# Kernel tuning notes

Hardware: AMD Instinct MI355X
Metric: run time of the kernel (lower is better)

Reference implementation:

```python
import jax, jax.numpy as jnp
import numpy as np

SEQ = 4096
EMBED = 1024


def setup_inputs() -> dict:
    key = jax.random.key(0)
    k1, k2 = jax.random.split(key)
    x = jax.random.normal(k1, (SEQ, EMBED), dtype=jnp.float32)
    # torch Linear(embed, 3*embed): store transposed weight so y = x @ W + b
    W = jax.random.normal(k2, (EMBED, 3 * EMBED), dtype=jnp.float32) * (1.0 / np.sqrt(EMBED))
    b = jnp.zeros((3 * EMBED,), dtype=jnp.float32)
    return {"x": x, "W": W, "b": b}


def reference(x, W, b):
    # QKV projection: [S, 3E] -> chunk along features
    qkv = x @ W + b
    q, k, v = jnp.split(qkv, 3, axis=1)  # each [S, E]
    d = q.shape[-1]
    scale = jnp.sqrt(jnp.asarray(d, dtype=x.dtype))
    logits = (q @ k.T) / scale  # [S, S]
    S = q.shape[0]
    causal = jnp.triu(jnp.ones((S, S), dtype=bool), k=1)
    logits = jnp.where(causal, -jnp.inf, logits)
    w = jax.nn.softmax(logits, axis=1)
    return w @ v  # [S, E]
```

## Files before the change

### kernel.cpp

```cpp
#include <hip/hip_runtime.h>

typedef short s16x8 __attribute__((ext_vector_type(8)));
typedef unsigned short u16;
typedef u16 u16x8 __attribute__((ext_vector_type(8)));
typedef float f32x4 __attribute__((ext_vector_type(4)));

#define SEQ 4096
#define EMBED 1024
#define NQKV 3072

static __device__ __forceinline__ u16 f2bf(float f) {
  unsigned int u = __float_as_uint(f);
  u += 0x7fffu + ((u >> 16) & 1u);
  return (u16)(u >> 16);
}
static __device__ __forceinline__ float bf2f(u16 b) {
  return __uint_as_float(((unsigned int)b) << 16);
}

static __device__ __forceinline__ f32x4 mfma16(s16x8 a, s16x8 b, f32x4 c) {
  return __builtin_amdgcn_mfma_f32_16x16x32_bf16(a, b, c, 0, 0, 0);
}

static __device__ __forceinline__ void gl2lds(const u16* g, u16* l) {
  __builtin_amdgcn_global_load_lds(
      (const __attribute__((address_space(1))) unsigned int*)g,
      (__attribute__((address_space(3))) unsigned int*)l, 16, 0, 0);
}

#define WAITVM(n) asm volatile("s_waitcnt vmcnt(" #n ")" ::: "memory")
#define LGKM0 asm volatile("s_waitcnt lgkmcnt(0)" ::: "memory")
#define BAR() asm volatile("s_waitcnt lgkmcnt(0)\n\ts_barrier" ::: "memory")

__global__ __launch_bounds__(256) void conv_x(const float* __restrict__ x,
                                              u16* __restrict__ xbf) {
  const size_t base = ((size_t)blockIdx.x * 256 + threadIdx.x) * 16;
  u16 tmp[16];
#pragma unroll
  for (int p = 0; p < 4; ++p) {
    float4 v = *reinterpret_cast<const float4*>(&x[base + p * 4]);
    tmp[p * 4 + 0] = f2bf(v.x); tmp[p * 4 + 1] = f2bf(v.y);
    tmp[p * 4 + 2] = f2bf(v.z); tmp[p * 4 + 3] = f2bf(v.w);
  }
  *reinterpret_cast<u16x8*>(&xbf[base]) = *reinterpret_cast<u16x8*>(&tmp[0]);
  *reinterpret_cast<u16x8*>(&xbf[base + 8]) = *reinterpret_cast<u16x8*>(&tmp[8]);
}

__global__ __launch_bounds__(256) void conv_wT(const float* __restrict__ W,
                                               u16* __restrict__ wT) {
  __shared__ u16 t[64][72];
  const int n0 = blockIdx.x * 64;
  const int k0 = blockIdx.y * 64;
  const int tid = threadIdx.x;
  const int rr = tid >> 3, c8 = (tid & 7) * 8;
#pragma unroll
  for (int p = 0; p < 2; ++p) {
    int r = p * 32 + rr;
    float4 a = *reinterpret_cast<const float4*>(&W[(size_t)(k0 + r) * NQKV + n0 + c8]);
    float4 b = *reinterpret_cast<const float4*>(&W[(size_t)(k0 + r) * NQKV + n0 + c8 + 4]);
    t[r][c8 + 0] = f2bf(a.x); t[r][c8 + 1] = f2bf(a.y);
    t[r][c8 + 2] = f2bf(a.z); t[r][c8 + 3] = f2bf(a.w);
    t[r][c8 + 4] = f2bf(b.x); t[r][c8 + 5] = f2bf(b.y);
    t[r][c8 + 6] = f2bf(b.z); t[r][c8 + 7] = f2bf(b.w);
  }
  __syncthreads();
#pragma unroll
  for (int p = 0; p < 2; ++p) {
    int c = p * 32 + rr;
    u16x8 v;
#pragma unroll
    for (int j = 0; j < 8; ++j) v[j] = t[c8 + j][c];
    *reinterpret_cast<u16x8*>(&wT[(size_t)(n0 + c) * EMBED + k0 + c8]) = v;
  }
}

#define GSTAGE(dst, srcbase, stride)                                          \
  {                                                                           \
    _Pragma("unroll") for (int c_ = 0; c_ < 4; ++c_) {                        \
      gl2lds((srcbase) + (size_t)((c_ * 4 + w) * 8 + srow) * (stride) + scol, \
             (dst) + (c_ * 4 + w) * 512);                                     \
    }                                                                         \
  }

__global__ __launch_bounds__(256) void qkv_gemm(const u16* __restrict__ xbf,
                                                const u16* __restrict__ wT,
                                                const float* __restrict__ bias,
                                                u16* __restrict__ qkv) {
  __shared__ u16 As[2][8192];
  __shared__ u16 Bs[2][8192];
  const int b = blockIdx.x;
  const int bs = (b & 7) * 96 + (b >> 3);
  const int bm = bs / 24, bn = bs % 24;
  const int m0 = bm * 128, n0 = bn * 128;
  const int tid = threadIdx.x;
  const int w = tid >> 6, l = tid & 63;
  const int wr = (w >> 1) * 64, wc = (w & 1) * 64;
  const int lg = l >> 4, lr = l & 15;
  const int srow = l >> 3;
  const int scol = ((l & 7) ^ (srow & 7)) << 3;

  f32x4 acc[4][4];
#pragma unroll
  for (int i = 0; i < 4; ++i)
#pragma unroll
    for (int j = 0; j < 4; ++j) acc[i][j] = (f32x4){0.f, 0.f, 0.f, 0.f};

  const u16* xa = xbf + (size_t)m0 * EMBED;
  const u16* wb = wT + (size_t)n0 * EMBED;

  GSTAGE(As[0], xa, EMBED);
  GSTAGE(Bs[0], wb, EMBED);

  for (int t = 0; t < 16; ++t) {
    const int cur = t & 1, nx = cur ^ 1;
    if (t < 15) {
      LGKM0;
      GSTAGE(As[nx], xa + (t + 1) * 64, EMBED);
      GSTAGE(Bs[nx], wb + (t + 1) * 64, EMBED);
      WAITVM(8);
    } else {
      WAITVM(0);
    }
    BAR();
#pragma unroll
    for (int kk = 0; kk < 2; ++kk) {
      const int csw = (kk * 32 + lg * 8) ^ ((lr & 7) << 3);
      s16x8 af[4], bfr[4];
#pragma unroll
      for (int mb = 0; mb < 4; ++mb)
        af[mb] = *reinterpret_cast<const s16x8*>(&As[cur][(wr + mb * 16 + lr) * 64 + csw]);
#pragma unroll
      for (int nb = 0; nb < 4; ++nb)
        bfr[nb] = *reinterpret_cast<const s16x8*>(&Bs[cur][(wc + nb * 16 + lr) * 64 + csw]);
#pragma unroll
      for (int mb = 0; mb < 4; ++mb)
#pragma unroll
        for (int nb = 0; nb < 4; ++nb)
          acc[mb][nb] = mfma16(af[mb], bfr[nb], acc[mb][nb]);
    }
    BAR();
  }

#pragma unroll
  for (int mb = 0; mb < 4; ++mb)
#pragma unroll
    for (int nb = 0; nb < 4; ++nb) {
      const int col = n0 + wc + nb * 16 + lr;
      const float bv = bias[col];
#pragma unroll
      for (int e = 0; e < 4; ++e) {
        const int row = m0 + wr + mb * 16 + lg * 4 + e;
        qkv[(size_t)row * NQKV + col] = f2bf(acc[mb][nb][e] + bv);
      }
    }
}

__global__ __launch_bounds__(256) void v_transpose(const u16* __restrict__ qkv,
                                                   u16* __restrict__ vT) {
  __shared__ u16 t[64][72];
  const int s0 = blockIdx.x * 64;
  const int c0 = blockIdx.y * 64;
  const int tid = threadIdx.x;
  const int rr = tid >> 3, c8 = (tid & 7) * 8;
#pragma unroll
  for (int p = 0; p < 2; ++p) {
    int r = p * 32 + rr;
    *reinterpret_cast<u16x8*>(&t[r][c8]) =
        *reinterpret_cast<const u16x8*>(&qkv[(size_t)(s0 + r) * NQKV + 2 * EMBED + c0 + c8]);
  }
  __syncthreads();
#pragma unroll
  for (int p = 0; p < 2; ++p) {
    int c = p * 32 + rr;
    u16x8 v;
#pragma unroll
    for (int j = 0; j < 8; ++j) v[j] = t[c8 + j][c];
    *reinterpret_cast<u16x8*>(&vT[(size_t)(c0 + c) * SEQ + s0 + c8]) = v;
  }
}

__global__ __launch_bounds__(256) void s_gemm(const u16* __restrict__ qkv,
                                              u16* __restrict__ Sp) {
  __shared__ u16 As[2][8192];
  __shared__ u16 Bs[2][8192];
  const int b = blockIdx.x;
  const int bs = (b & 7) * 66 + (b >> 3);
  int mt = 0, cum = 0;
  while (cum + mt + 1 <= bs) { cum += mt + 1; ++mt; }
  const int nt = bs - cum;
  const int m0 = mt * 128, n0 = nt * 128;
  const int tid = threadIdx.x;
  const int w = tid >> 6, l = tid & 63;
  const int wr = (w >> 1) * 64, wc = (w & 1) * 64;
  const int lg = l >> 4, lr = l & 15;
  const int srow = l >> 3;
  const int scol = ((l & 7) ^ (srow & 7)) << 3;

  f32x4 acc[4][4];
#pragma unroll
  for (int i = 0; i < 4; ++i)
#pragma unroll
    for (int j = 0; j < 4; ++j) acc[i][j] = (f32x4){0.f, 0.f, 0.f, 0.f};

  const u16* qa = qkv + (size_t)m0 * NQKV;
  const u16* kb = qkv + (size_t)n0 * NQKV + EMBED;

  GSTAGE(As[0], qa, NQKV);
  GSTAGE(Bs[0], kb, NQKV);

  for (int t = 0; t < 16; ++t) {
    const int cur = t & 1, nx = cur ^ 1;
    if (t < 15) {
      LGKM0;
      GSTAGE(As[nx], qa + (t + 1) * 64, NQKV);
      GSTAGE(Bs[nx], kb + (t + 1) * 64, NQKV);
      WAITVM(8);
    } else {
      WAITVM(0);
    }
    BAR();
#pragma unroll
    for (int kk = 0; kk < 2; ++kk) {
      const int csw = (kk * 32 + lg * 8) ^ ((lr & 7) << 3);
      s16x8 af[4], bfr[4];
#pragma unroll
      for (int mb = 0; mb < 4; ++mb)
        af[mb] = *reinterpret_cast<const s16x8*>(&As[cur][(wr + mb * 16 + lr) * 64 + csw]);
#pragma unroll
      for (int nb = 0; nb < 4; ++nb)
        bfr[nb] = *reinterpret_cast<const s16x8*>(&Bs[cur][(wc + nb * 16 + lr) * 64 + csw]);
#pragma unroll
      for (int mb = 0; mb < 4; ++mb)
#pragma unroll
        for (int nb = 0; nb < 4; ++nb)
          acc[mb][nb] = mfma16(af[mb], bfr[nb], acc[mb][nb]);
    }
    BAR();
  }

  u16* base = Sp + (size_t)bs * 16384;
#pragma unroll
  for (int mb = 0; mb < 4; ++mb)
#pragma unroll
    for (int nb = 0; nb < 4; ++nb) {
      const int cn = wc + nb * 16 + lr;
#pragma unroll
      for (int e = 0; e < 4; ++e) {
        const int rm = wr + mb * 16 + lg * 4 + e;
        base[rm * 128 + cn] = f2bf(acc[mb][nb][e]);
      }
    }
}

__global__ __launch_bounds__(256) void softmax_rows(u16* __restrict__ Sp) {
  __shared__ float red[8];
  const int bid = blockIdx.x;
  const int tid = threadIdx.x;
  const int w = tid >> 6, l = tid & 63;
  const float NEG = -3.0e38f;

  for (int half = 0; half < 2; ++half) {
    const int r = half ? (4095 - bid) : bid;
    const int mt = r >> 7, rr = r & 127;
    const int Lp = (mt + 1) << 7;
    const size_t tri = (size_t)mt * (mt + 1) / 2;

    float v[16];
    float mx = NEG;
#pragma unroll
    for (int s = 0; s < 2; ++s) {
      const int j = tid * 8 + s * 2048;
      if (j < Lp) {
        const u16* p = Sp + (tri + (j >> 7)) * 16384 + rr * 128 + (j & 127);
        u16x8 xv = *reinterpret_cast<const u16x8*>(p);
#pragma unroll
        for (int e = 0; e < 8; ++e) {
          float f = (j + e <= r) ? bf2f(xv[e]) * 0.03125f : NEG;
          v[s * 8 + e] = f;
          mx = fmaxf(mx, f);
        }
      } else {
#pragma unroll
        for (int e = 0; e < 8; ++e) v[s * 8 + e] = NEG;
      }
    }
#pragma unroll
    for (int off = 32; off >= 1; off >>= 1) mx = fmaxf(mx, __shfl_xor(mx, off, 64));
    if (l == 0) red[w] = mx;
    __syncthreads();
    mx = fmaxf(fmaxf(red[0], red[1]), fmaxf(red[2], red[3]));

    float sum = 0.f;
#pragma unroll
    for (int i = 0; i < 16; ++i) {
      float e = __expf(v[i] - mx);
      v[i] = e;
      sum += e;
    }
#pragma unroll
    for (int off = 32; off >= 1; off >>= 1) sum += __shfl_xor(sum, off, 64);
    if (l == 0) red[4 + w] = sum;
    __syncthreads();
    sum = red[4] + red[5] + red[6] + red[7];
    const float inv = 1.f / sum;

#pragma unroll
    for (int s = 0; s < 2; ++s) {
      const int j = tid * 8 + s * 2048;
      if (j < Lp) {
        u16x8 pk;
#pragma unroll
        for (int e = 0; e < 8; ++e) pk[e] = f2bf(v[s * 8 + e] * inv);
        *reinterpret_cast<u16x8*>(Sp + (tri + (j >> 7)) * 16384 + rr * 128 + (j & 127)) = pk;
      }
    }
    __syncthreads();
  }
}

__global__ __launch_bounds__(256) void pv_gemm(const u16* __restrict__ Sp,
                                               const u16* __restrict__ vT,
                                               float* __restrict__ out) {
  __shared__ u16 As[2][8192];
  __shared__ u16 Bs[2][8192];
  const int nt = blockIdx.y;
  int s81 = blockIdx.x;
  int mt = 0, cum = 0, ls = 0;
  for (;;) {
    const int ns = (mt + 8) >> 3;
    if (s81 < cum + ns) { ls = s81 - cum; break; }
    cum += ns; ++mt;
  }
  const int m0 = mt * 128, n0 = nt * 128;
  const int k0 = ls * 1024;
  const int kext = (mt + 1) * 128;
  const int kend = (k0 + 1024 < kext) ? (k0 + 1024) : kext;
  const int ksteps = (kend - k0) >> 6;
  const size_t tri = (size_t)mt * (mt + 1) / 2;

  const int tid = threadIdx.x;
  const int w = tid >> 6, l = tid & 63;
  const int wr = (w >> 1) * 64, wc = (w & 1) * 64;
  const int lg = l >> 4, lr = l & 15;
  const int srow = l >> 3;
  const int scol = ((l & 7) ^ (srow & 7)) << 3;

  f32x4 acc[4][4];
#pragma unroll
  for (int i = 0; i < 4; ++i)
#pragma unroll
    for (int j = 0; j < 4; ++j) acc[i][j] = (f32x4){0.f, 0.f, 0.f, 0.f};

#define PA_SRC(t) (Sp + (tri + ((k0 + (t)*64) >> 7)) * 16384 + ((k0 + (t)*64) & 127))
#define PB_SRC(t) (vT + (size_t)n0 * SEQ + k0 + (t)*64)

  GSTAGE(As[0], PA_SRC(0), 128);
  GSTAGE(Bs[0], PB_SRC(0), SEQ);

  for (int t = 0; t < ksteps; ++t) {
    const int cur = t & 1, nx = cur ^ 1;
    if (t + 1 < ksteps) {
      LGKM0;
      GSTAGE(As[nx], PA_SRC(t + 1), 128);
      GSTAGE(Bs[nx], PB_SRC(t + 1), SEQ);
      WAITVM(8);
    } else {
      WAITVM(0);
    }
    BAR();
#pragma unroll
    for (int kk = 0; kk < 2; ++kk) {
      const int csw = (kk * 32 + lg * 8) ^ ((lr & 7) << 3);
      s16x8 af[4], bfr[4];
#pragma unroll
      for (int mb = 0; mb < 4; ++mb)
        af[mb] = *reinterpret_cast<const s16x8*>(&As[cur][(wr + mb * 16 + lr) * 64 + csw]);
#pragma unroll
      for (int nb = 0; nb < 4; ++nb)
        bfr[nb] = *reinterpret_cast<const s16x8*>(&Bs[cur][(wc + nb * 16 + lr) * 64 + csw]);
#pragma unroll
      for (int mb = 0; mb < 4; ++mb)
#pragma unroll
        for (int nb = 0; nb < 4; ++nb)
          acc[mb][nb] = mfma16(af[mb], bfr[nb], acc[mb][nb]);
    }
    BAR();
  }
#undef PA_SRC
#undef PB_SRC

#pragma unroll
  for (int mb = 0; mb < 4; ++mb)
#pragma unroll
    for (int nb = 0; nb < 4; ++nb) {
      const int col = n0 + wc + nb * 16 + lr;
#pragma unroll
      for (int e = 0; e < 4; ++e) {
        const int row = m0 + wr + mb * 16 + lg * 4 + e;
        unsafeAtomicAdd(&out[(size_t)row * EMBED + col], acc[mb][nb][e]);
      }
    }
}

__global__ __launch_bounds__(512) void attn_fb(const u16* __restrict__ qkv,
                                               const u16* __restrict__ vT,
                                               float* __restrict__ out) {
  __shared__ u16 q_lds[16][1032];
  __shared__ u16 kv_lds[8][3][2048];
  __shared__ u16 p_lds[16][136];
  __shared__ float redmax[8][16];
  __shared__ float redsum[8][16];
  const int bid = blockIdx.x;
  const int tid = threadIdx.x;
  const int w = tid >> 6, l = tid & 63;
  const int lg = l >> 4, lr = l & 15;

  const int sr = l >> 4;
  const int scb = (l & 15) * 16;
  const int scolA = ((scb ^ (sr << 4)) >> 1);
  const int scolB = ((scb ^ ((4 + sr) << 4)) >> 1);
  int boff[4];
#pragma unroll
  for (int kk = 0; kk < 4; ++kk)
    boff[kk] = lr * 256 + ((kk * 64 + lg * 16) ^ ((lr & 7) << 4));

  u16* kvb[3] = {&kv_lds[w][0][0], &kv_lds[w][1][0], &kv_lds[w][2][0]};

#define STAGE_K(dc, bufp)                                                     \
  {                                                                           \
    LGKM0;                                                                    \
    const u16* g0 = qkv + (size_t)(kb + w * 16 + sr) * NQKV + EMBED + (dc) * 128; \
    gl2lds(g0 + scolA, (bufp));                                               \
    gl2lds(g0 + 4 * NQKV + scolB, (bufp) + 512);                              \
    gl2lds(g0 + 8 * NQKV + scolA, (bufp) + 1024);                             \
    gl2lds(g0 + 12 * NQKV + scolB, (bufp) + 1536);                            \
  }
#define STAGE_V(j, bufp)                                                      \
  {                                                                           \
    LGKM0;                                                                    \
    const u16* g0 = vT + (size_t)((j) * 128 + w * 16 + sr) * SEQ + kb;        \
    gl2lds(g0 + scolA, (bufp));                                               \
    gl2lds(g0 + 4 * SEQ + scolB, (bufp) + 512);                               \
    gl2lds(g0 + 8 * SEQ + scolA, (bufp) + 1024);                              \
    gl2lds(g0 + 12 * SEQ + scolB, (bufp) + 1536);                             \
  }

  const int qb = bid * 16;
  __syncthreads();
#pragma unroll
  for (int p = 0; p < 4; ++p) {
    int idx = p * 512 + tid;
    int r = idx >> 7, c = (idx & 127) * 8;
    *reinterpret_cast<u16x8*>(&q_lds[r][c]) =
        *reinterpret_cast<const u16x8*>(&qkv[(size_t)(qb + r) * NQKV + c]);
  }
  __syncthreads();
  s16x8 qf[32];
#pragma unroll
  for (int kk = 0; kk < 32; ++kk)
    qf[kk] = *reinterpret_cast<const s16x8*>(&q_lds[lr][kk * 32 + lg * 8]);

  f32x4 o_acc[8];
#pragma unroll
  for (int j = 0; j < 8; ++j) o_acc[j] = (f32x4){0.f, 0.f, 0.f, 0.f};
  float m_st[4], l_st[4];
#pragma unroll
  for (int e = 0; e < 4; ++e) { m_st[e] = -__builtin_inff(); l_st[e] = 0.f; }

  const int n_it = (qb >> 7) + 1;
  for (int it = 0; it < n_it; ++it) {
    const int kb = it << 7;
    const int kcol = kb + w * 16 + lr;

    f32x4 s = (f32x4){0.f, 0.f, 0.f, 0.f};
    STAGE_K(0, kvb[0]);
    STAGE_K(1, kvb[1]);
#pragma unroll
    for (int dc = 0; dc < 8; ++dc) {
      if (dc < 6) {
        STAGE_K(dc + 2, kvb[(dc + 2) % 3]);
      } else if (dc == 6) {
        STAGE_V(0, kvb[2]);
      } else {
        STAGE_V(1, kvb[0]);
      }
      WAITVM(8);
      u16* cur = kvb[dc % 3];
#pragma unroll
      for (int kk = 0; kk < 4; ++kk) {
        s16x8 bfr = *reinterpret_cast<const s16x8*>((const char*)cur + boff[kk]);
        s = mfma16(qf[dc * 4 + kk], bfr, s);
      }
    }

    float sv[4], mx[4];
#pragma unroll
    for (int e = 0; e < 4; ++e) {
      float v = s[e] * 0.03125f;
      sv[e] = (kcol > qb + lg * 4 + e) ? -__builtin_inff() : v;
      mx[e] = sv[e];
    }
#pragma unroll
    for (int off = 1; off < 16; off <<= 1)
#pragma unroll
      for (int e = 0; e < 4; ++e) mx[e] = fmaxf(mx[e], __shfl_xor(mx[e], off, 64));
    if (lr == 0) {
#pragma unroll
      for (int e = 0; e < 4; ++e) redmax[w][lg * 4 + e] = mx[e];
    }
    BAR();

    float m_new[4], sc[4], pv[4], rs[4];
#pragma unroll
    for (int e = 0; e < 4; ++e) {
      float m = m_st[e];
#pragma unroll
      for (int ww = 0; ww < 8; ++ww) m = fmaxf(m, redmax[ww][lg * 4 + e]);
      m_new[e] = m;
      sc[e] = __expf(m_st[e] - m);
      pv[e] = __expf(sv[e] - m);
      rs[e] = pv[e];
    }
#pragma unroll
    for (int off = 1; off < 16; off <<= 1)
#pragma unroll
      for (int e = 0; e < 4; ++e) rs[e] += __shfl_xor(rs[e], off, 64);
    if (lr == 0) {
#pragma unroll
      for (int e = 0; e < 4; ++e) redsum[w][lg * 4 + e] = rs[e];
    }
#pragma unroll
    for (int e = 0; e < 4; ++e) p_lds[lg * 4 + e][w * 16 + lr] = f2bf(pv[e]);
    BAR();

#pragma unroll
    for (int e = 0; e < 4; ++e) {
      float a2 = l_st[e] * sc[e];
#pragma unroll
      for (int ww = 0; ww < 8; ++ww) a2 += redsum[ww][lg * 4 + e];
      l_st[e] = a2;
      m_st[e] = m_new[e];
    }
#pragma unroll
    for (int j = 0; j < 8; ++j)
#pragma unroll
      for (int e = 0; e < 4; ++e) o_acc[j][e] *= sc[e];

    s16x8 pa[4];
#pragma unroll
    for (int kk = 0; kk < 4; ++kk)
      pa[kk] = *reinterpret_cast<const s16x8*>(&p_lds[lr][kk * 32 + lg * 8]);

#pragma unroll
    for (int j = 0; j < 8; ++j) {
      if (j < 6) {
        STAGE_V(j + 2, kvb[(j + 4) % 3]);
        WAITVM(8);
      } else if (j == 6) {
        WAITVM(4);
      } else {
        WAITVM(0);
      }
      u16* cur = kvb[(j + 2) % 3];
#pragma unroll
      for (int kk = 0; kk < 4; ++kk) {
        s16x8 bfr = *reinterpret_cast<const s16x8*>((const char*)cur + boff[kk]);
        o_acc[j] = mfma16(pa[kk], bfr, o_acc[j]);
      }
    }
  }

#pragma unroll
  for (int j = 0; j < 8; ++j) {
    const int col = j * 128 + w * 16 + lr;
#pragma unroll
    for (int e = 0; e < 4; ++e)
      out[(size_t)(qb + lg * 4 + e) * EMBED + col] = o_acc[j][e] / l_st[e];
  }
#undef STAGE_K
#undef STAGE_V
}

extern "C" void kernel_launch(void* const* d_in, const int* in_sizes, int n_in,
                              void* d_out, int out_size, void* d_ws, size_t ws_size,
                              hipStream_t stream) {
  (void)in_sizes; (void)n_in; (void)out_size;
  const float* x = (const float*)d_in[0];
  const float* W = (const float*)d_in[1];
  const float* bias = (const float*)d_in[2];
  float* out = (float*)d_out;

  u16* qkv = (u16*)d_ws;
  u16* vT = qkv + (size_t)SEQ * NQKV;
  u16* xbf = vT;
  u16* wT = (u16*)d_out;
  u16* Sp = (u16*)((char*)d_ws + (32u << 20));

  const size_t need = (32u << 20) + (size_t)528 * 16384 * 2;

  conv_x<<<(SEQ * EMBED) / (256 * 16), 256, 0, stream>>>(x, xbf);
  conv_wT<<<dim3(NQKV / 64, EMBED / 64), 256, 0, stream>>>(W, wT);
  qkv_gemm<<<(SEQ / 128) * (NQKV / 128), 256, 0, stream>>>(xbf, wT, bias, qkv);
  v_transpose<<<dim3(SEQ / 64, EMBED / 64), 256, 0, stream>>>(qkv, vT);

  if (ws_size >= need) {
    s_gemm<<<528, 256, 0, stream>>>(qkv, Sp);
    softmax_rows<<<2048, 256, 0, stream>>>(Sp);
    hipMemsetAsync(d_out, 0, (size_t)SEQ * EMBED * sizeof(float), stream);
    pv_gemm<<<dim3(80, 8), 256, 0, stream>>>(Sp, vT, out);
  } else {
    attn_fb<<<SEQ / 16, 512, 0, stream>>>(qkv, vT, out);
  }
}
```

Baseline: 168.8 us.

## Replace split-K PV GEMM with stream-K work partitioning across 512 blocks

The fixed 80x8 split-K grid for the causal P·V GEMM becomes a stream-K kernel. The 8448 total k-steps are split evenly across 512 blocks, each walking a contiguous range of (m-tile, n-tile, k-step) work and atomically flushing its accumulators whenever the tile changes. This targets the load imbalance from triangular tiles of unequal k-length. The cost is more partial-tile atomic flushes and extra index bookkeeping inside the loop, and the block-index swizzle is meant to spread work across XCDs.

```diff
diff --git a/kernel.cpp b/kernel.cpp
--- a/kernel.cpp
+++ b/kernel.cpp
@@ -318,25 +318,15 @@
   }
 }
 
-__global__ __launch_bounds__(256) void pv_gemm(const u16* __restrict__ Sp,
-                                               const u16* __restrict__ vT,
-                                               float* __restrict__ out) {
+__global__ __launch_bounds__(256) void pv_streamk(const u16* __restrict__ Sp,
+                                                  const u16* __restrict__ vT,
+                                                  float* __restrict__ out) {
   __shared__ u16 As[2][8192];
   __shared__ u16 Bs[2][8192];
-  const int nt = blockIdx.y;
-  int s81 = blockIdx.x;
-  int mt = 0, cum = 0, ls = 0;
-  for (;;) {
-    const int ns = (mt + 8) >> 3;
-    if (s81 < cum + ns) { ls = s81 - cum; break; }
-    cum += ns; ++mt;
-  }
-  const int m0 = mt * 128, n0 = nt * 128;
-  const int k0 = ls * 1024;
-  const int kext = (mt + 1) * 128;
-  const int kend = (k0 + 1024 < kext) ? (k0 + 1024) : kext;
-  const int ksteps = (kend - k0) >> 6;
-  const size_t tri = (size_t)mt * (mt + 1) / 2;
+  const int b = blockIdx.x;
+  const int bs = (b & 7) * 64 + (b >> 3);
+  const int start = (33 * bs) >> 1;
+  const int end = (33 * (bs + 1)) >> 1;
 
   const int tid = threadIdx.x;
   const int w = tid >> 6, l = tid & 63;
@@ -345,24 +335,39 @@
   const int srow = l >> 3;
   const int scol = ((l & 7) ^ (srow & 7)) << 3;
 
+  int mt = 0;
+  while (8 * (mt + 1) * (mt + 2) <= start) ++mt;
+  int kc = 2 * (mt + 1);
+  int rem = start - 8 * mt * (mt + 1);
+  int nt = rem / kc, ks = rem % kc;
+
+#define PV_STAGE(MT, NT, KS, buf)                                             \
+  {                                                                           \
+    LGKM0;                                                                    \
+    const u16* asrc = Sp + ((size_t)((MT) * ((MT) + 1) / 2) + ((KS) >> 1)) * 16384 + ((KS)&1) * 64; \
+    const u16* bsrc = vT + (size_t)(NT)*128 * SEQ + (KS)*64;                  \
+    GSTAGE(As[buf], asrc, 128);                                               \
+    GSTAGE(Bs[buf], bsrc, SEQ);                                               \
+  }
+
   f32x4 acc[4][4];
 #pragma unroll
   for (int i = 0; i < 4; ++i)
 #pragma unroll
     for (int j = 0; j < 4; ++j) acc[i][j] = (f32x4){0.f, 0.f, 0.f, 0.f};
 
-#define PA_SRC(t) (Sp + (tri + ((k0 + (t)*64) >> 7)) * 16384 + ((k0 + (t)*64) & 127))
-#define PB_SRC(t) (vT + (size_t)n0 * SEQ + k0 + (t)*64)
-
-  GSTAGE(As[0], PA_SRC(0), 128);
-  GSTAGE(Bs[0], PB_SRC(0), SEQ);
-
-  for (int t = 0; t < ksteps; ++t) {
-    const int cur = t & 1, nx = cur ^ 1;
-    if (t + 1 < ksteps) {
-      LGKM0;
-      GSTAGE(As[nx], PA_SRC(t + 1), 128);
-      GSTAGE(Bs[nx], PB_SRC(t + 1), SEQ);
+  PV_STAGE(mt, nt, ks, 0);
+  int cur = 0;
+
+  for (int it = start; it < end; ++it) {
+    int nmt = mt, nnt = nt, nks = ks + 1, nkc = kc;
+    if (nks == kc) {
+      nks = 0; nnt = nt + 1;
+      if (nnt == 8) { nnt = 0; nmt = mt + 1; nkc = kc + 2; }
+    }
+    const bool last = (it + 1 == end);
+    if (!last) {
+      PV_STAGE(nmt, nnt, nks, cur ^ 1);
       WAITVM(8);
     } else {
       WAITVM(0);
@@ -385,21 +390,24 @@
           acc[mb][nb] = mfma16(af[mb], bfr[nb], acc[mb][nb]);
     }
     BAR();
-  }
-#undef PA_SRC
-#undef PB_SRC
-
-#pragma unroll
-  for (int mb = 0; mb < 4; ++mb)
-#pragma unroll
-    for (int nb = 0; nb < 4; ++nb) {
-      const int col = n0 + wc + nb * 16 + lr;
-#pragma unroll
-      for (int e = 0; e < 4; ++e) {
-        const int row = m0 + wr + mb * 16 + lg * 4 + e;
-        unsafeAtomicAdd(&out[(size_t)row * EMBED + col], acc[mb][nb][e]);
-      }
-    }
+
+    if (last || nnt != nt || nmt != mt) {
+#pragma unroll
+      for (int mb = 0; mb < 4; ++mb)
+#pragma unroll
+        for (int nb = 0; nb < 4; ++nb) {
+          const int col = nt * 128 + wc + nb * 16 + lr;
+#pragma unroll
+          for (int e = 0; e < 4; ++e) {
+            const int row = mt * 128 + wr + mb * 16 + lg * 4 + e;
+            unsafeAtomicAdd(&out[(size_t)row * EMBED + col], acc[mb][nb][e]);
+            acc[mb][nb][e] = 0.f;
+          }
+        }
+    }
+    mt = nmt; nt = nnt; ks = nks; kc = nkc; cur ^= 1;
+  }
+#undef PV_STAGE
 }
 
 __global__ __launch_bounds__(512) void attn_fb(const u16* __restrict__ qkv,
@@ -607,7 +615,7 @@
     s_gemm<<<528, 256, 0, stream>>>(qkv, Sp);
     softmax_rows<<<2048, 256, 0, stream>>>(Sp);
     hipMemsetAsync(d_out, 0, (size_t)SEQ * EMBED * sizeof(float), stream);
-    pv_gemm<<<dim3(80, 8), 256, 0, stream>>>(Sp, vT, out);
+    pv_streamk<<<512, 256, 0, stream>>>(Sp, vT, out);
   } else {
     attn_fb<<<SEQ / 16, 512, 0, stream>>>(qkv, vT, out);
   }
```

After: 173.3 us. 1.03x slower.

## Halve GEMM K-tile to 32 to cut LDS usage; fold softmax scale into S epilogue

Applied to the files above, without the earlier changes.

All three GEMM kernels now stage 32-wide K slices instead of 64, which halves the shared-memory footprint per block and lets more blocks fit per CU. The XOR swizzle is dropped because each 64-byte row is now read contiguously. The price is twice as many barriers and pipeline iterations, and possible LDS bank conflicts without the swizzle. Separately, the 1/32 logit scale moves from the softmax load into the S GEMM epilogue before rounding to bf16.

```diff
diff --git a/kernel.cpp b/kernel.cpp
--- a/kernel.cpp
+++ b/kernel.cpp
@@ -74,20 +74,33 @@
   }
 }
 
-#define GSTAGE(dst, srcbase, stride)                                          \
+#define GSTAGE32(dst, srcbase, stride)                                        \
   {                                                                           \
-    _Pragma("unroll") for (int c_ = 0; c_ < 4; ++c_) {                        \
-      gl2lds((srcbase) + (size_t)((c_ * 4 + w) * 8 + srow) * (stride) + scol, \
-             (dst) + (c_ * 4 + w) * 512);                                     \
+    _Pragma("unroll") for (int p_ = 0; p_ < 2; ++p_) {                        \
+      gl2lds((srcbase) + (size_t)(p_ * 64 + w * 16 + (l >> 2)) * (stride) +   \
+                 (l & 3) * 8,                                                 \
+             (dst) + p_ * 2048 + w * 512);                                    \
     }                                                                         \
+  }
+
+#define MFMA_STEP(Acur, Bcur)                                                 \
+  {                                                                           \
+    s16x8 af[4], bfr[4];                                                      \
+    _Pragma("unroll") for (int mb = 0; mb < 4; ++mb)                          \
+        af[mb] = *reinterpret_cast<const s16x8*>(&(Acur)[(wr + mb * 16 + lr) * 32 + lg * 8]); \
+    _Pragma("unroll") for (int nb = 0; nb < 4; ++nb)                          \
+        bfr[nb] = *reinterpret_cast<const s16x8*>(&(Bcur)[(wc + nb * 16 + lr) * 32 + lg * 8]); \
+    _Pragma("unroll") for (int mb = 0; mb < 4; ++mb)                          \
+        _Pragma("unroll") for (int nb = 0; nb < 4; ++nb)                      \
+            acc[mb][nb] = mfma16(af[mb], bfr[nb], acc[mb][nb]);               \
   }
 
 __global__ __launch_bounds__(256) void qkv_gemm(const u16* __restrict__ xbf,
                                                 const u16* __restrict__ wT,
                                                 const float* __restrict__ bias,
                                                 u16* __restrict__ qkv) {
-  __shared__ u16 As[2][8192];
-  __shared__ u16 Bs[2][8192];
+  __shared__ u16 As[2][4096];
+  __shared__ u16 Bs[2][4096];
   const int b = blockIdx.x;
   const int bs = (b & 7) * 96 + (b >> 3);
   const int bm = bs / 24, bn = bs % 24;
@@ -96,8 +109,6 @@
   const int w = tid >> 6, l = tid & 63;
   const int wr = (w >> 1) * 64, wc = (w & 1) * 64;
   const int lg = l >> 4, lr = l & 15;
-  const int srow = l >> 3;
-  const int scol = ((l & 7) ^ (srow & 7)) << 3;
 
   f32x4 acc[4][4];
 #pragma unroll
@@ -108,36 +119,21 @@
   const u16* xa = xbf + (size_t)m0 * EMBED;
   const u16* wb = wT + (size_t)n0 * EMBED;
 
-  GSTAGE(As[0], xa, EMBED);
-  GSTAGE(Bs[0], wb, EMBED);
-
-  for (int t = 0; t < 16; ++t) {
+  GSTAGE32(As[0], xa, EMBED);
+  GSTAGE32(Bs[0], wb, EMBED);
+
+  for (int t = 0; t < 32; ++t) {
     const int cur = t & 1, nx = cur ^ 1;
-    if (t < 15) {
+    if (t < 31) {
       LGKM0;
-      GSTAGE(As[nx], xa + (t + 1) * 64, EMBED);
-      GSTAGE(Bs[nx], wb + (t + 1) * 64, EMBED);
-      WAITVM(8);
+      GSTAGE32(As[nx], xa + (t + 1) * 32, EMBED);
+      GSTAGE32(Bs[nx], wb + (t + 1) * 32, EMBED);
+      WAITVM(4);
     } else {
       WAITVM(0);
     }
     BAR();
-#pragma unroll
-    for (int kk = 0; kk < 2; ++kk) {
-      const int csw = (kk * 32 + lg * 8) ^ ((lr & 7) << 3);
-      s16x8 af[4], bfr[4];
-#pragma unroll
-      for (int mb = 0; mb < 4; ++mb)
-        af[mb] = *reinterpret_cast<const s16x8*>(&As[cur][(wr + mb * 16 + lr) * 64 + csw]);
-#pragma unroll
-      for (int nb = 0; nb < 4; ++nb)
-        bfr[nb] = *reinterpret_cast<const s16x8*>(&Bs[cur][(wc + nb * 16 + lr) * 64 + csw]);
-#pragma unroll
-      for (int mb = 0; mb < 4; ++mb)
-#pragma unroll
-        for (int nb = 0; nb < 4; ++nb)
-          acc[mb][nb] = mfma16(af[mb], bfr[nb], acc[mb][nb]);
-    }
+    MFMA_STEP(As[cur], Bs[cur]);
     BAR();
   }
 
@@ -181,8 +177,8 @@
 
 __global__ __launch_bounds__(256) void s_gemm(const u16* __restrict__ qkv,
                                               u16* __restrict__ Sp) {
-  __shared__ u16 As[2][8192];
-  __shared__ u16 Bs[2][8192];
+  __shared__ u16 As[2][4096];
+  __shared__ u16 Bs[2][4096];
   const int b = blockIdx.x;
   const int bs = (b & 7) * 66 + (b >> 3);
   int mt = 0, cum = 0;
@@ -193,8 +189,6 @@
   const int w = tid >> 6, l = tid & 63;
   const int wr = (w >> 1) * 64, wc = (w & 1) * 64;
   const int lg = l >> 4, lr = l & 15;
-  const int srow = l >> 3;
-  const int scol = ((l & 7) ^ (srow & 7)) << 3;
 
   f32x4 acc[4][4];
 #pragma unroll
@@ -205,36 +199,21 @@
   const u16* qa = qkv + (size_t)m0 * NQKV;
   const u16* kb = qkv + (size_t)n0 * NQKV + EMBED;
 
-  GSTAGE(As[0], qa, NQKV);
-  GSTAGE(Bs[0], kb, NQKV);
-
-  for (int t = 0; t < 16; ++t) {
+  GSTAGE32(As[0], qa, NQKV);
+  GSTAGE32(Bs[0], kb, NQKV);
+
+  for (int t = 0; t < 32; ++t) {
     const int cur = t & 1, nx = cur ^ 1;
-    if (t < 15) {
+    if (t < 31) {
       LGKM0;
-      GSTAGE(As[nx], qa + (t + 1) * 64, NQKV);
-      GSTAGE(Bs[nx], kb + (t + 1) * 64, NQKV);
-      WAITVM(8);
+      GSTAGE32(As[nx], qa + (t + 1) * 32, NQKV);
+      GSTAGE32(Bs[nx], kb + (t + 1) * 32, NQKV);
+      WAITVM(4);
     } else {
       WAITVM(0);
     }
     BAR();
-#pragma unroll
-    for (int kk = 0; kk < 2; ++kk) {
-      const int csw = (kk * 32 + lg * 8) ^ ((lr & 7) << 3);
-      s16x8 af[4], bfr[4];
-#pragma unroll
-      for (int mb = 0; mb < 4; ++mb)
-        af[mb] = *reinterpret_cast<const s16x8*>(&As[cur][(wr + mb * 16 + lr) * 64 + csw]);
-#pragma unroll
-      for (int nb = 0; nb < 4; ++nb)
-        bfr[nb] = *reinterpret_cast<const s16x8*>(&Bs[cur][(wc + nb * 16 + lr) * 64 + csw]);
-#pragma unroll
-      for (int mb = 0; mb < 4; ++mb)
-#pragma unroll
-        for (int nb = 0; nb < 4; ++nb)
-          acc[mb][nb] = mfma16(af[mb], bfr[nb], acc[mb][nb]);
-    }
+    MFMA_STEP(As[cur], Bs[cur]);
     BAR();
   }
 
@@ -247,7 +226,7 @@
 #pragma unroll
       for (int e = 0; e < 4; ++e) {
         const int rm = wr + mb * 16 + lg * 4 + e;
-        base[rm * 128 + cn] = f2bf(acc[mb][nb][e]);
+        base[rm * 128 + cn] = f2bf(acc[mb][nb][e] * 0.03125f);
       }
     }
 }
@@ -275,7 +254,7 @@
         u16x8 xv = *reinterpret_cast<const u16x8*>(p);
 #pragma unroll
         for (int e = 0; e < 8; ++e) {
-          float f = (j + e <= r) ? bf2f(xv[e]) * 0.03125f : NEG;
+          float f = (j + e <= r) ? bf2f(xv[e]) : NEG;
           v[s * 8 + e] = f;
           mx = fmaxf(mx, f);
         }
@@ -321,8 +300,8 @@
 __global__ __launch_bounds__(256) void pv_gemm(const u16* __restrict__ Sp,
                                                const u16* __restrict__ vT,
                                                float* __restrict__ out) {
-  __shared__ u16 As[2][8192];
-  __shared__ u16 Bs[2][8192];
+  __shared__ u16 As[2][4096];
+  __shared__ u16 Bs[2][4096];
   const int nt = blockIdx.y;
   int s81 = blockIdx.x;
   int mt = 0, cum = 0, ls = 0;
@@ -335,15 +314,13 @@
   const int k0 = ls * 1024;
   const int kext = (mt + 1) * 128;
   const int kend = (k0 + 1024 < kext) ? (k0 + 1024) : kext;
-  const int ksteps = (kend - k0) >> 6;
+  const int ksteps = (kend - k0) >> 5;
   const size_t tri = (size_t)mt * (mt + 1) / 2;
 
   const int tid = threadIdx.x;
   const int w = tid >> 6, l = tid & 63;
   const int wr = (w >> 1) * 64, wc = (w & 1) * 64;
   const int lg = l >> 4, lr = l & 15;
-  const int srow = l >> 3;
-  const int scol = ((l & 7) ^ (srow & 7)) << 3;
 
   f32x4 acc[4][4];
 #pragma unroll
@@ -351,39 +328,24 @@
 #pragma unroll
     for (int j = 0; j < 4; ++j) acc[i][j] = (f32x4){0.f, 0.f, 0.f, 0.f};
 
-#define PA_SRC(t) (Sp + (tri + ((k0 + (t)*64) >> 7)) * 16384 + ((k0 + (t)*64) & 127))
-#define PB_SRC(t) (vT + (size_t)n0 * SEQ + k0 + (t)*64)
-
-  GSTAGE(As[0], PA_SRC(0), 128);
-  GSTAGE(Bs[0], PB_SRC(0), SEQ);
+#define PA_SRC(t) (Sp + (tri + ((k0 + (t)*32) >> 7)) * 16384 + ((k0 + (t)*32) & 127))
+#define PB_SRC(t) (vT + (size_t)n0 * SEQ + k0 + (t)*32)
+
+  GSTAGE32(As[0], PA_SRC(0), 128);
+  GSTAGE32(Bs[0], PB_SRC(0), SEQ);
 
   for (int t = 0; t < ksteps; ++t) {
     const int cur = t & 1, nx = cur ^ 1;
     if (t + 1 < ksteps) {
       LGKM0;
-      GSTAGE(As[nx], PA_SRC(t + 1), 128);
-      GSTAGE(Bs[nx], PB_SRC(t + 1), SEQ);
-      WAITVM(8);
+      GSTAGE32(As[nx], PA_SRC(t + 1), 128);
+      GSTAGE32(Bs[nx], PB_SRC(t + 1), SEQ);
+      WAITVM(4);
     } else {
       WAITVM(0);
     }
     BAR();
-#pragma unroll
-    for (int kk = 0; kk < 2; ++kk) {
-      const int csw = (kk * 32 + lg * 8) ^ ((lr & 7) << 3);
-      s16x8 af[4], bfr[4];
-#pragma unroll
-      for (int mb = 0; mb < 4; ++mb)
-        af[mb] = *reinterpret_cast<const s16x8*>(&As[cur][(wr + mb * 16 + lr) * 64 + csw]);
-#pragma unroll
-      for (int nb = 0; nb < 4; ++nb)
-        bfr[nb] = *reinterpret_cast<const s16x8*>(&Bs[cur][(wc + nb * 16 + lr) * 64 + csw]);
-#pragma unroll
-      for (int mb = 0; mb < 4; ++mb)
-#pragma unroll
-        for (int nb = 0; nb < 4; ++nb)
-          acc[mb][nb] = mfma16(af[mb], bfr[nb], acc[mb][nb]);
-    }
+    MFMA_STEP(As[cur], Bs[cur]);
     BAR();
   }
 #undef PA_SRC
```

New measurement: 158.0 us. -6.4%, faster.
